# Kernel tuning notes

Measured on AMD Instinct MI355X. Metric: run time of the kernel, lower is better.

The kernel has to match this reference:

```python
import jax, jax.numpy as jnp
import numpy as np

B, N, Z = 32, 8192, 1024


def setup_inputs() -> dict:
    key = jax.random.key(0)
    ks = jax.random.split(key, 11)
    def w(k, shape, fan_in):
        # kaiming-ish init scale for conv1d k=1
        return jax.random.normal(k, shape, dtype=jnp.float32) * (1.0 / np.sqrt(fan_in))
    return {
        "x": jax.random.normal(ks[0], (B, 3, N), dtype=jnp.float32),
        "W1": w(ks[1], (64, 3), 3),   "b1": jnp.zeros((64,), jnp.float32),
        "W2": w(ks[2], (128, 64), 64), "b2": jnp.zeros((128,), jnp.float32),
        "W3": w(ks[3], (256, 128), 128), "b3": jnp.zeros((256,), jnp.float32),
        "W4": w(ks[4], (256, 256), 256), "b4": jnp.zeros((256,), jnp.float32),
        "W5": w(ks[5], (Z, 256), 256),  "b5": jnp.zeros((Z,), jnp.float32),
    }


def _pointwise(x, W, b):
    # Conv1d with kernel_size=1 == per-point linear: [B,C,N] x [O,C] -> [B,O,N]
    return jnp.einsum('bcn,oc->bon', x, W) + b[None, :, None]


def reference(x, W1, b1, W2, b2, W3, b3, W4, b4, W5, b5):
    h = jax.nn.relu(_pointwise(x, W1, b1))
    h = jax.nn.relu(_pointwise(h, W2, b2))
    h = jax.nn.relu(_pointwise(h, W3, b3))
    h = jax.nn.relu(_pointwise(h, W4, b4))
    h = _pointwise(h, W5, b5)           # [B, Z, N]
    return jnp.max(h, axis=2)           # global max pool over points -> [B, Z]
```

## Files before the change

### kernel.cpp

```cpp
#include <hip/hip_runtime.h>
#include <math.h>

#define NB      32
#define NPTS    8192
#define TOTPTS  (NB * NPTS)

typedef unsigned short u16;
typedef unsigned int   u32;
typedef __attribute__((ext_vector_type(8))) short bf16x8;
typedef __attribute__((ext_vector_type(4))) float f32x4;

__device__ __forceinline__ u16 f2bf(float f) {
    u32 u = __float_as_uint(f);
    u = (u + 0x7fffu + ((u >> 16) & 1u)) >> 16;
    return (u16)u;
}
__device__ __forceinline__ u32 pk2(float a, float b) {
    return (u32)f2bf(a) | ((u32)f2bf(b) << 16);
}
__device__ __forceinline__ f32x4 MFMA(bf16x8 a, bf16x8 b, f32x4 c) {
    return __builtin_amdgcn_mfma_f32_16x16x32_bf16(a, b, c, 0, 0, 0);
}
template<int CTRL>
__device__ __forceinline__ float dpp_max(float v) {
    int t = __builtin_amdgcn_update_dpp(__float_as_int(v), __float_as_int(v),
                                        CTRL, 0xF, 0xF, false);
    return fmaxf(v, __int_as_float(t));
}
__device__ __forceinline__ float rowmax16(float v) {
    v = dpp_max<0xB1>(v);
    v = dpp_max<0x4E>(v);
    v = dpp_max<0x141>(v);
    v = dpp_max<0x140>(v);
    return v;
}
__device__ __forceinline__ void gload16(const void* g, void* l) {
    __builtin_amdgcn_global_load_lds(
        (const __attribute__((address_space(1))) unsigned int*)g,
        (__attribute__((address_space(3))) unsigned int*)l, 16, 0, 0);
}
template<int N> __device__ __forceinline__ void vwait() {
    if constexpr      (N == 0) asm volatile("s_waitcnt vmcnt(0)" ::: "memory");
    else if constexpr (N == 2) asm volatile("s_waitcnt vmcnt(2)" ::: "memory");
    else if constexpr (N == 4) asm volatile("s_waitcnt vmcnt(4)" ::: "memory");
    else                       asm volatile("s_waitcnt vmcnt(8)" ::: "memory");
}
__device__ __forceinline__ void pin(bf16x8& v) { asm volatile("" : "+v"(v)); }


__global__ __launch_bounds__(256) void k_pack(const float* __restrict__ W2,
        const float* __restrict__ W3, const float* __restrict__ W4,
        const float* __restrict__ W5, u16* __restrict__ dst) {
    int idx = blockIdx.x * 256 + threadIdx.x;
    if (idx >= 720 * 64) return;
    int lane = idx & 63, fr = idx >> 6;
    const float* W; int C, frl;
    if (fr < 16)       { W = W2; C = 64;  frl = fr;       }
    else if (fr < 80)  { W = W3; C = 128; frl = fr - 16;  }
    else if (fr < 208) { W = W4; C = 256; frl = fr - 80;  }
    else               { W = W5; C = 256; frl = fr - 208; }
    int KF = C >> 5;
    int nf = frl / KF, kf = frl % KF;
    int o = nf * 16 + (lane & 15), c = kf * 32 + (lane >> 4) * 8;
    const float* s = W + (size_t)o * C + c;
    u32 out[4];
    #pragma unroll
    for (int j = 0; j < 4; ++j) out[j] = pk2(s[2 * j], s[2 * j + 1]);
    *(uint4*)((char*)dst + (size_t)idx * 16) = make_uint4(out[0], out[1], out[2], out[3]);
}

__global__ __launch_bounds__(512, 2) void k_fuse(const float* __restrict__ x,
        const float* __restrict__ W1, const float* __restrict__ b1,
        const u16* __restrict__ W2p, const float* __restrict__ b2,
        const u16* __restrict__ W3p, const float* __restrict__ b3,
        const u16* __restrict__ W4p, const float* __restrict__ b4,
        u16* __restrict__ H4, int pt0, int tpb) {
    __shared__ char regA[65536];
    __shared__ char regB[32768];
    const int tid = threadIdx.x, lane = tid & 63, w = tid >> 6;
    const int l15 = lane & 15, q = lane >> 4;
    const int qterm = ((q >> 1) * 16 + l15) * 16 + (q & 1) * 8;
    const int pl = tid & 127;
    const int c4 = tid >> 7;

    bf16x8 W2r[2], W3r[2][4], W4r[2][8];
    #pragma unroll
    for (int kf = 0; kf < 2; ++kf) {
        W2r[kf] = *(const bf16x8*)((const char*)W2p + (size_t)(w * 2 + kf) * 1024 + lane * 16);
        pin(W2r[kf]);
    }
    #pragma unroll
    for (int n = 0; n < 2; ++n)
        #pragma unroll
        for (int kf = 0; kf < 4; ++kf) {
            W3r[n][kf] = *(const bf16x8*)((const char*)W3p +
                           (size_t)((w * 2 + n) * 4 + kf) * 1024 + lane * 16);
            pin(W3r[n][kf]);
        }
    #pragma unroll
    for (int n = 0; n < 2; ++n)
        #pragma unroll
        for (int kf = 0; kf < 8; ++kf) {
            W4r[n][kf] = *(const bf16x8*)((const char*)W4p +
                           (size_t)((w * 2 + n) * 8 + kf) * 1024 + lane * 16);
            pin(W4r[n][kf]);
        }
    const f32x4 b2v = *(const f32x4*)(b2 + w * 16 + q * 4);
    f32x4 b3v[2], b4v[2];
    #pragma unroll
    for (int n = 0; n < 2; ++n) {
        b3v[n] = *(const f32x4*)(b3 + (w * 2 + n) * 16 + q * 4);
        b4v[n] = *(const f32x4*)(b4 + (w * 2 + n) * 16 + q * 4);
    }

    const int tile0 = blockIdx.x * tpb;
    float x0, x1, x2;
    {
        int ptg = pt0 + tile0 * 128 + pl;
        const float* xb = x + (size_t)(ptg >> 13) * 3 * NPTS + (ptg & 8191);
        x0 = xb[0]; x1 = xb[NPTS]; x2 = xb[2 * NPTS];
    }

    for (int it = 0; it < tpb; ++it) {
        const int tile = tile0 + it;
        {
            u32 pk4[8];
            #pragma unroll
            for (int i = 0; i < 8; ++i) {
                int o0 = c4 * 16 + 2 * i, o1 = o0 + 1;
                float a0 = fmaxf(b1[o0] + W1[o0*3]*x0 + W1[o0*3+1]*x1 + W1[o0*3+2]*x2, 0.f);
                float a1 = fmaxf(b1[o1] + W1[o1*3]*x0 + W1[o1*3+1]*x1 + W1[o1*3+2]*x2, 0.f);
                pk4[i] = pk2(a0, a1);
            }
            char* rowp = regA + pl * 128;
            const int swz = (pl & 7) << 4;
            *(uint4*)(rowp + ((c4 * 32) ^ swz))      = make_uint4(pk4[0], pk4[1], pk4[2], pk4[3]);
            *(uint4*)(rowp + ((c4 * 32 + 16) ^ swz)) = make_uint4(pk4[4], pk4[5], pk4[6], pk4[7]);
        }
        __syncthreads();
        #pragma unroll
        for (int pf = 0; pf < 8; ++pf) {
            const int r2 = pf * 16 + l15;
            const char* rb = regA + r2 * 128;
            const int rsw = (r2 & 7) << 4;
            bf16x8 B0 = *(const bf16x8*)(rb + ((q * 16) ^ rsw));
            bf16x8 B1 = *(const bf16x8*)(rb + ((64 + q * 16) ^ rsw));
            f32x4 a = b2v;
            a = MFMA(W2r[0], B0, a);
            a = MFMA(W2r[1], B1, a);
            u32 d0 = pk2(fmaxf(a[0], 0.f), fmaxf(a[1], 0.f));
            u32 d1 = pk2(fmaxf(a[2], 0.f), fmaxf(a[3], 0.f));
            *(uint2*)(regB + (pf * 4 + (w >> 1)) * 1024 + (w & 1) * 512 + qterm)
                = make_uint2(d0, d1);
        }
        __syncthreads();
        #pragma unroll
        for (int pf = 0; pf < 8; ++pf) {
            bf16x8 B[4];
            #pragma unroll
            for (int kf = 0; kf < 4; ++kf)
                B[kf] = *(const bf16x8*)(regB + (pf * 4 + kf) * 1024 + lane * 16);
            f32x4 a0 = b3v[0], a1 = b3v[1];
            #pragma unroll
            for (int kf = 0; kf < 4; ++kf) {
                a0 = MFMA(W3r[0][kf], B[kf], a0);
                a1 = MFMA(W3r[1][kf], B[kf], a1);
            }
            char* db = regA + (pf * 8 + w) * 1024;
            *(uint2*)(db + qterm)       = make_uint2(pk2(fmaxf(a0[0],0.f), fmaxf(a0[1],0.f)),
                                                     pk2(fmaxf(a0[2],0.f), fmaxf(a0[3],0.f)));
            *(uint2*)(db + 512 + qterm) = make_uint2(pk2(fmaxf(a1[0],0.f), fmaxf(a1[1],0.f)),
                                                     pk2(fmaxf(a1[2],0.f), fmaxf(a1[3],0.f)));
        }
        __syncthreads();
        #pragma unroll
        for (int pf = 0; pf < 8; ++pf) {
            bf16x8 B[8];
            #pragma unroll
            for (int kf = 0; kf < 8; ++kf)
                B[kf] = *(const bf16x8*)(regA + (pf * 8 + kf) * 1024 + lane * 16);
            f32x4 a0 = b4v[0], a1 = b4v[1];
            #pragma unroll
            for (int kf = 0; kf < 8; ++kf) {
                a0 = MFMA(W4r[0][kf], B[kf], a0);
                a1 = MFMA(W4r[1][kf], B[kf], a1);
            }
            char* db = (char*)H4 + ((size_t)(tile * 8 + pf) * 8 + w) * 1024;
            *(uint2*)(db + qterm)       = make_uint2(pk2(fmaxf(a0[0],0.f), fmaxf(a0[1],0.f)),
                                                     pk2(fmaxf(a0[2],0.f), fmaxf(a0[3],0.f)));
            *(uint2*)(db + 512 + qterm) = make_uint2(pk2(fmaxf(a1[0],0.f), fmaxf(a1[1],0.f)),
                                                     pk2(fmaxf(a1[2],0.f), fmaxf(a1[3],0.f)));
        }
        if (it + 1 < tpb) {
            int ptg = pt0 + (tile + 1) * 128 + pl;
            const float* xb = x + (size_t)(ptg >> 13) * 3 * NPTS + (ptg & 8191);
            x0 = xb[0]; x1 = xb[NPTS]; x2 = xb[2 * NPTS];
        }
        __syncthreads();
    }
}

__global__ __launch_bounds__(512, 2) void k_l5(const u16* __restrict__ Hin,
        const u16* __restrict__ Wp, const float* __restrict__ b5,
        float* __restrict__ parts, int slot0) {
    constexpr int BUFB = 16384;
    constexpr int STEPS = 32;
    __shared__ char ldsB[3 * BUFB];
    const int tid = threadIdx.x, lane = tid & 63, w = tid >> 6;
    const int l15 = lane & 15, q = lane >> 4;
    const int zsl = blockIdx.x & 1, pgrp = blockIdx.x >> 1;
    const int pfb = pgrp * 64;

    bf16x8 W[4][8];
    {
        const char* wb = (const char*)Wp + (size_t)(zsl * 32 + w * 4) * 8 * 1024;
        #pragma unroll
        for (int nf = 0; nf < 4; ++nf)
            #pragma unroll
            for (int kf = 0; kf < 8; ++kf)
                W[nf][kf] = *(const bf16x8*)(wb + (size_t)(nf * 8 + kf) * 1024 + lane * 16);
    }
    f32x4 vmax[4];
    #pragma unroll
    for (int nf = 0; nf < 4; ++nf)
        #pragma unroll
        for (int r = 0; r < 4; ++r) vmax[nf][r] = -3.402823466e38f;

    auto stage = [&](int t, int bsel) {
        const char* g = (const char*)Hin + ((size_t)(pfb + t * 2) * 8) * 1024
                        + w * 2048 + lane * 16;
        char* l = ldsB + bsel * BUFB + w * 2048;
        gload16(g, l);
        gload16(g + 1024, l + 1024);
    };
    stage(0, 0);
    stage(1, 1);
    int bufc = 0;
    for (int t = 0; t < STEPS; ++t) {
        if (t + 1 < STEPS) vwait<2>(); else vwait<0>();
        __builtin_amdgcn_sched_barrier(0);
        __builtin_amdgcn_s_barrier();
        const char* bp = ldsB + bufc * BUFB;
        #pragma unroll
        for (int p = 0; p < 2; ++p) {
            f32x4 acc[4];
            #pragma unroll
            for (int nf = 0; nf < 4; ++nf)
                #pragma unroll
                for (int r = 0; r < 4; ++r) acc[nf][r] = 0.f;
            #pragma unroll
            for (int kf = 0; kf < 8; ++kf) {
                bf16x8 B = *(const bf16x8*)(bp + (size_t)(p * 8 + kf) * 1024 + lane * 16);
                #pragma unroll
                for (int nf = 0; nf < 4; ++nf) acc[nf] = MFMA(W[nf][kf], B, acc[nf]);
            }
            #pragma unroll
            for (int nf = 0; nf < 4; ++nf)
                #pragma unroll
                for (int r = 0; r < 4; ++r)
                    vmax[nf][r] = fmaxf(vmax[nf][r], acc[nf][r]);
        }
        if (t + 2 < STEPS) {
            int b2 = bufc + 2; if (b2 >= 3) b2 -= 3;
            stage(t + 2, b2);
        }
        ++bufc; if (bufc == 3) bufc = 0;
    }
    const int zb = zsl * 512 + w * 64;
    float* dst = parts + (size_t)(slot0 + pgrp) * 1024 + zb;
    #pragma unroll
    for (int nf = 0; nf < 4; ++nf)
        #pragma unroll
        for (int r = 0; r < 4; ++r) {
            float m = rowmax16(vmax[nf][r]);
            if (l15 == nf * 4 + r) {
                int zi = nf * 16 + q * 4 + r;
                dst[zi] = m + b5[zb + zi];
            }
        }
}

__global__ __launch_bounds__(256) void k_red(const float* __restrict__ parts,
                                             float* __restrict__ out) {
    int i = blockIdx.x * 256 + threadIdx.x;
    int b = i >> 10, z = i & 1023;
    float m = -3.402823466e38f;
    #pragma unroll
    for (int s = 0; s < 8; ++s)
        m = fmaxf(m, parts[((size_t)b * 8 + s) * 1024 + z]);
    out[i] = m;
}

extern "C" void kernel_launch(void* const* d_in, const int* in_sizes, int n_in,
                              void* d_out, int out_size, void* d_ws, size_t ws_size,
                              hipStream_t stream) {
    const float* x  = (const float*)d_in[0];
    const float* W1 = (const float*)d_in[1]; const float* b1 = (const float*)d_in[2];
    const float* W2 = (const float*)d_in[3]; const float* b2 = (const float*)d_in[4];
    const float* W3 = (const float*)d_in[5]; const float* b3 = (const float*)d_in[6];
    const float* W4 = (const float*)d_in[7]; const float* b4 = (const float*)d_in[8];
    const float* W5 = (const float*)d_in[9]; const float* b5 = (const float*)d_in[10];

    u16* wsW = (u16*)d_ws;
    const u16* W2p = (const u16*)((char*)d_ws + 0);
    const u16* W3p = (const u16*)((char*)d_ws + 16 * 1024);
    const u16* W4p = (const u16*)((char*)d_ws + 80 * 1024);
    const u16* W5p = (const u16*)((char*)d_ws + 208 * 1024);
    float* parts   = (float*)((char*)d_ws + 786432);
    char* Hbase    = (char*)d_ws + 786432 + 2097152;

    int NCH = 1;
    while (NCH < 32) {
        size_t npc = (size_t)TOTPTS / NCH;
        if (786432 + 2097152 + npc * 512 <= ws_size) break;
        NCH *= 2;
    }
    const size_t npts_c = (size_t)TOTPTS / NCH;
    char* HB = Hbase;

    k_pack<<<dim3(180), dim3(256), 0, stream>>>(W2, W3, W4, W5, wsW);

    const int ntiles = (int)(npts_c / 128);
    const int nblk   = (ntiles >= 256) ? 256 : ntiles;
    const int tpb    = ntiles / nblk;
    const int npc_pf = (int)(npts_c / 16);
    for (int c = 0; c < NCH; ++c) {
        int pt0   = (int)(c * npts_c);
        int slot0 = (int)((c * npts_c) >> 10);
        k_fuse<<<dim3(nblk), dim3(512), 0, stream>>>(
            x, W1, b1, W2p, b2, W3p, b3, W4p, b4, (u16*)HB, pt0, tpb);
        k_l5<<<dim3(2 * (npc_pf / 64)), dim3(512), 0, stream>>>(
            (const u16*)HB, W5p, b5, parts, slot0);
    }
    k_red<<<dim3(128), dim3(256), 0, stream>>>(parts, (float*)d_out);
}
```

Baseline: 164.4 us.

## Switch layer-5 GEMM to 32x32x16 MFMA with matching H4 and W5 layouts

Layer 5 now uses the 32x32x16 bf16 MFMA instead of 16x16x32. The W5 packing, the H4 intermediate layout written by k_fuse, the staging addresses, and the final max reduction epilogue are all changed to fit the 32-wide fragment layout. The larger MFMA shape raises operand reuse per instruction and cuts LDS B-fragment reads per output tile. The cost is a more complex epilogue that needs cross-half shuffles, plus the chance of layout-index mistakes.

```diff
diff --git a/kernel.cpp b/kernel.cpp
--- a/kernel.cpp
+++ b/kernel.cpp
@@ -9,6 +9,7 @@
 typedef unsigned int   u32;
 typedef __attribute__((ext_vector_type(8))) short bf16x8;
 typedef __attribute__((ext_vector_type(4))) float f32x4;
+typedef __attribute__((ext_vector_type(16))) float f32x16;
 
 __device__ __forceinline__ u16 f2bf(float f) {
     u32 u = __float_as_uint(f);
@@ -20,6 +21,9 @@
 }
 __device__ __forceinline__ f32x4 MFMA(bf16x8 a, bf16x8 b, f32x4 c) {
     return __builtin_amdgcn_mfma_f32_16x16x32_bf16(a, b, c, 0, 0, 0);
+}
+__device__ __forceinline__ f32x16 MFMA32(bf16x8 a, bf16x8 b, f32x16 c) {
+    return __builtin_amdgcn_mfma_f32_32x32x16_bf16(a, b, c, 0, 0, 0);
 }
 template<int CTRL>
 __device__ __forceinline__ float dpp_max(float v) {
@@ -42,8 +46,7 @@
 template<int N> __device__ __forceinline__ void vwait() {
     if constexpr      (N == 0) asm volatile("s_waitcnt vmcnt(0)" ::: "memory");
     else if constexpr (N == 2) asm volatile("s_waitcnt vmcnt(2)" ::: "memory");
-    else if constexpr (N == 4) asm volatile("s_waitcnt vmcnt(4)" ::: "memory");
-    else                       asm volatile("s_waitcnt vmcnt(8)" ::: "memory");
+    else                       asm volatile("s_waitcnt vmcnt(4)" ::: "memory");
 }
 __device__ __forceinline__ void pin(bf16x8& v) { asm volatile("" : "+v"(v)); }
 
@@ -54,14 +57,23 @@
     int idx = blockIdx.x * 256 + threadIdx.x;
     if (idx >= 720 * 64) return;
     int lane = idx & 63, fr = idx >> 6;
-    const float* W; int C, frl;
-    if (fr < 16)       { W = W2; C = 64;  frl = fr;       }
-    else if (fr < 80)  { W = W3; C = 128; frl = fr - 16;  }
-    else if (fr < 208) { W = W4; C = 256; frl = fr - 80;  }
-    else               { W = W5; C = 256; frl = fr - 208; }
-    int KF = C >> 5;
-    int nf = frl / KF, kf = frl % KF;
-    int o = nf * 16 + (lane & 15), c = kf * 32 + (lane >> 4) * 8;
+    const float* W; int C, o, c;
+    if (fr < 208) {
+        int frl;
+        if (fr < 16)      { W = W2; C = 64;  frl = fr;      }
+        else if (fr < 80) { W = W3; C = 128; frl = fr - 16; }
+        else              { W = W4; C = 256; frl = fr - 80; }
+        int KF = C >> 5;
+        int nf = frl / KF, kf = frl % KF;
+        o = nf * 16 + (lane & 15);
+        c = kf * 32 + (lane >> 4) * 8;
+    } else {
+        int frl = fr - 208;
+        int nf = frl >> 4, kf = frl & 15;
+        W = W5; C = 256;
+        o = nf * 32 + (lane & 31);
+        c = kf * 16 + (lane >> 5) * 8;
+    }
     const float* s = W + (size_t)o * C + c;
     u32 out[4];
     #pragma unroll
@@ -185,11 +197,14 @@
                 a0 = MFMA(W4r[0][kf], B[kf], a0);
                 a1 = MFMA(W4r[1][kf], B[kf], a1);
             }
-            char* db = (char*)H4 + ((size_t)(tile * 8 + pf) * 8 + w) * 1024;
-            *(uint2*)(db + qterm)       = make_uint2(pk2(fmaxf(a0[0],0.f), fmaxf(a0[1],0.f)),
-                                                     pk2(fmaxf(a0[2],0.f), fmaxf(a0[3],0.f)));
-            *(uint2*)(db + 512 + qterm) = make_uint2(pk2(fmaxf(a1[0],0.f), fmaxf(a1[1],0.f)),
-                                                     pk2(fmaxf(a1[2],0.f), fmaxf(a1[3],0.f)));
+            const size_t pf32 = (size_t)tile * 4 + (pf >> 1);
+            const int lterm = ((q >> 1) * 32 + (pf & 1) * 16 + l15) * 16 + (q & 1) * 8;
+            char* d0p = (char*)H4 + (pf32 * 16 + (w * 2 + 0)) * 1024 + lterm;
+            char* d1p = (char*)H4 + (pf32 * 16 + (w * 2 + 1)) * 1024 + lterm;
+            *(uint2*)d0p = make_uint2(pk2(fmaxf(a0[0],0.f), fmaxf(a0[1],0.f)),
+                                      pk2(fmaxf(a0[2],0.f), fmaxf(a0[3],0.f)));
+            *(uint2*)d1p = make_uint2(pk2(fmaxf(a1[0],0.f), fmaxf(a1[1],0.f)),
+                                      pk2(fmaxf(a1[2],0.f), fmaxf(a1[3],0.f)));
         }
         if (it + 1 < tpb) {
             int ptg = pt0 + (tile + 1) * 128 + pl;
@@ -207,28 +222,24 @@
     constexpr int STEPS = 32;
     __shared__ char ldsB[3 * BUFB];
     const int tid = threadIdx.x, lane = tid & 63, w = tid >> 6;
-    const int l15 = lane & 15, q = lane >> 4;
     const int zsl = blockIdx.x & 1, pgrp = blockIdx.x >> 1;
-    const int pfb = pgrp * 64;
-
-    bf16x8 W[4][8];
+    const int pfb = pgrp * 32;
+
+    bf16x8 W[2][16];
     {
-        const char* wb = (const char*)Wp + (size_t)(zsl * 32 + w * 4) * 8 * 1024;
-        #pragma unroll
-        for (int nf = 0; nf < 4; ++nf)
-            #pragma unroll
-            for (int kf = 0; kf < 8; ++kf)
-                W[nf][kf] = *(const bf16x8*)(wb + (size_t)(nf * 8 + kf) * 1024 + lane * 16);
-    }
-    f32x4 vmax[4];
-    #pragma unroll
-    for (int nf = 0; nf < 4; ++nf)
-        #pragma unroll
-        for (int r = 0; r < 4; ++r) vmax[nf][r] = -3.402823466e38f;
+        const char* wb = (const char*)Wp + (size_t)(zsl * 16 + w * 2) * 16 * 1024;
+        #pragma unroll
+        for (int n = 0; n < 2; ++n)
+            #pragma unroll
+            for (int kf = 0; kf < 16; ++kf)
+                W[n][kf] = *(const bf16x8*)(wb + (size_t)(n * 16 + kf) * 1024 + lane * 16);
+    }
+    f32x16 vmax0, vmax1;
+    #pragma unroll
+    for (int r = 0; r < 16; ++r) { vmax0[r] = -3.402823466e38f; vmax1[r] = -3.402823466e38f; }
 
     auto stage = [&](int t, int bsel) {
-        const char* g = (const char*)Hin + ((size_t)(pfb + t * 2) * 8) * 1024
-                        + w * 2048 + lane * 16;
+        const char* g = (const char*)Hin + (size_t)(pfb + t) * 16384 + w * 2048 + lane * 16;
         char* l = ldsB + bsel * BUFB + w * 2048;
         gload16(g, l);
         gload16(g + 1024, l + 1024);
@@ -241,24 +252,19 @@
         __builtin_amdgcn_sched_barrier(0);
         __builtin_amdgcn_s_barrier();
         const char* bp = ldsB + bufc * BUFB;
-        #pragma unroll
-        for (int p = 0; p < 2; ++p) {
-            f32x4 acc[4];
-            #pragma unroll
-            for (int nf = 0; nf < 4; ++nf)
-                #pragma unroll
-                for (int r = 0; r < 4; ++r) acc[nf][r] = 0.f;
-            #pragma unroll
-            for (int kf = 0; kf < 8; ++kf) {
-                bf16x8 B = *(const bf16x8*)(bp + (size_t)(p * 8 + kf) * 1024 + lane * 16);
-                #pragma unroll
-                for (int nf = 0; nf < 4; ++nf) acc[nf] = MFMA(W[nf][kf], B, acc[nf]);
-            }
-            #pragma unroll
-            for (int nf = 0; nf < 4; ++nf)
-                #pragma unroll
-                for (int r = 0; r < 4; ++r)
-                    vmax[nf][r] = fmaxf(vmax[nf][r], acc[nf][r]);
+        f32x16 acc0, acc1;
+        #pragma unroll
+        for (int r = 0; r < 16; ++r) { acc0[r] = 0.f; acc1[r] = 0.f; }
+        #pragma unroll
+        for (int kf = 0; kf < 16; ++kf) {
+            bf16x8 B = *(const bf16x8*)(bp + (size_t)kf * 1024 + lane * 16);
+            acc0 = MFMA32(W[0][kf], B, acc0);
+            acc1 = MFMA32(W[1][kf], B, acc1);
+        }
+        #pragma unroll
+        for (int r = 0; r < 16; ++r) {
+            vmax0[r] = fmaxf(vmax0[r], acc0[r]);
+            vmax1[r] = fmaxf(vmax1[r], acc1[r]);
         }
         if (t + 2 < STEPS) {
             int b2 = bufc + 2; if (b2 >= 3) b2 -= 3;
@@ -267,17 +273,19 @@
         ++bufc; if (bufc == 3) bufc = 0;
     }
     const int zb = zsl * 512 + w * 64;
-    float* dst = parts + (size_t)(slot0 + pgrp) * 1024 + zb;
-    #pragma unroll
-    for (int nf = 0; nf < 4; ++nf)
-        #pragma unroll
-        for (int r = 0; r < 4; ++r) {
-            float m = rowmax16(vmax[nf][r]);
-            if (l15 == nf * 4 + r) {
-                int zi = nf * 16 + q * 4 + r;
-                dst[zi] = m + b5[zb + zi];
-            }
-        }
+    float mywr = -3.402823466e38f;
+    #pragma unroll
+    for (int r = 0; r < 16; ++r) {
+        float m0 = rowmax16(vmax0[r]);
+        m0 = fmaxf(m0, __shfl_xor(m0, 16, 64));
+        if ((lane & 31) == r) mywr = m0;
+        float m1 = rowmax16(vmax1[r]);
+        m1 = fmaxf(m1, __shfl_xor(m1, 16, 64));
+        if ((lane & 31) == 16 + r) mywr = m1;
+    }
+    const int r_ = lane & 15;
+    const int zloc = zb + ((lane >> 4) & 1) * 32 + (r_ & 3) + 8 * (r_ >> 2) + 4 * (lane >> 5);
+    parts[(size_t)(slot0 + pgrp) * 1024 + zloc] = mywr + b5[zloc];
 }
 
 __global__ __launch_bounds__(256) void k_red(const float* __restrict__ parts,
@@ -323,13 +331,12 @@
     const int ntiles = (int)(npts_c / 128);
     const int nblk   = (ntiles >= 256) ? 256 : ntiles;
     const int tpb    = ntiles / nblk;
-    const int npc_pf = (int)(npts_c / 16);
     for (int c = 0; c < NCH; ++c) {
         int pt0   = (int)(c * npts_c);
         int slot0 = (int)((c * npts_c) >> 10);
         k_fuse<<<dim3(nblk), dim3(512), 0, stream>>>(
             x, W1, b1, W2p, b2, W3p, b3, W4p, b4, (u16*)HB, pt0, tpb);
-        k_l5<<<dim3(2 * (npc_pf / 64)), dim3(512), 0, stream>>>(
+        k_l5<<<dim3(2 * (int)(npts_c / 1024)), dim3(512), 0, stream>>>(
             (const u16*)HB, W5p, b5, parts, slot0);
     }
     k_red<<<dim3(128), dim3(256), 0, stream>>>(parts, (float*)d_out);
```

Result: slower. 180.1 us (+9.6%).

## Give each wave a private double-buffered LDS stage in k_l5 and drop block barriers

Applied to the files above, without the earlier changes.

The layer-5 kernel used to share triple-buffered LDS tiles across all 8 waves and synchronise them with a workgroup barrier on every step. Now each wave loads its own copy of each point fragment into a private 16KB double buffer, so only per-wave vmcnt waits remain. Work per step drops to one fragment, with twice as many steps. It also pins the weight fragments to AGPRs, lowers launch bounds to one block per CU, and remaps block indices so the two z-slices of a point group run close together. In exchange, every wave now fetches the same data separately, which is eight times the global/L2 traffic for H4, and occupancy is halved.

```diff
diff --git a/kernel.cpp b/kernel.cpp
--- a/kernel.cpp
+++ b/kernel.cpp
@@ -45,7 +45,8 @@
     else if constexpr (N == 4) asm volatile("s_waitcnt vmcnt(4)" ::: "memory");
     else                       asm volatile("s_waitcnt vmcnt(8)" ::: "memory");
 }
-__device__ __forceinline__ void pin(bf16x8& v) { asm volatile("" : "+v"(v)); }
+__device__ __forceinline__ void pin(bf16x8& v)  { asm volatile("" : "+v"(v)); }
+__device__ __forceinline__ void pinA(bf16x8& v) { asm volatile("" : "+a"(v)); }
 
 
 __global__ __launch_bounds__(256) void k_pack(const float* __restrict__ W2,
@@ -200,16 +201,17 @@
     }
 }
 
-__global__ __launch_bounds__(512, 2) void k_l5(const u16* __restrict__ Hin,
+__global__ __launch_bounds__(512, 1) void k_l5(const u16* __restrict__ Hin,
         const u16* __restrict__ Wp, const float* __restrict__ b5,
         float* __restrict__ parts, int slot0) {
-    constexpr int BUFB = 16384;
-    constexpr int STEPS = 32;
-    __shared__ char ldsB[3 * BUFB];
+    constexpr int STEPS = 64;
+    __shared__ char ldsB[131072];
     const int tid = threadIdx.x, lane = tid & 63, w = tid >> 6;
     const int l15 = lane & 15, q = lane >> 4;
-    const int zsl = blockIdx.x & 1, pgrp = blockIdx.x >> 1;
-    const int pfb = pgrp * 64;
+    const int bid  = blockIdx.x;
+    const int zsl  = (bid >> 3) & 1;
+    const int pgrp = (bid & 7) | ((bid >> 4) << 3);
+    const int pfb  = pgrp * 64;
 
     bf16x8 W[4][8];
     {
@@ -217,8 +219,10 @@
         #pragma unroll
         for (int nf = 0; nf < 4; ++nf)
             #pragma unroll
-            for (int kf = 0; kf < 8; ++kf)
+            for (int kf = 0; kf < 8; ++kf) {
                 W[nf][kf] = *(const bf16x8*)(wb + (size_t)(nf * 8 + kf) * 1024 + lane * 16);
+                pinA(W[nf][kf]);
+            }
     }
     f32x4 vmax[4];
     #pragma unroll
@@ -226,45 +230,38 @@
         #pragma unroll
         for (int r = 0; r < 4; ++r) vmax[nf][r] = -3.402823466e38f;
 
+    char* myb = ldsB + w * 16384;
     auto stage = [&](int t, int bsel) {
-        const char* g = (const char*)Hin + ((size_t)(pfb + t * 2) * 8) * 1024
-                        + w * 2048 + lane * 16;
-        char* l = ldsB + bsel * BUFB + w * 2048;
-        gload16(g, l);
-        gload16(g + 1024, l + 1024);
+        const char* g = (const char*)Hin + ((size_t)(pfb + t) * 8) * 1024 + lane * 16;
+        char* l = myb + bsel * 8192;
+        #pragma unroll
+        for (int i = 0; i < 8; ++i)
+            gload16(g + i * 1024, l + i * 1024);
     };
     stage(0, 0);
     stage(1, 1);
-    int bufc = 0;
     for (int t = 0; t < STEPS; ++t) {
-        if (t + 1 < STEPS) vwait<2>(); else vwait<0>();
+        if (t < STEPS - 1) vwait<8>(); else vwait<0>();
         __builtin_amdgcn_sched_barrier(0);
-        __builtin_amdgcn_s_barrier();
-        const char* bp = ldsB + bufc * BUFB;
-        #pragma unroll
-        for (int p = 0; p < 2; ++p) {
-            f32x4 acc[4];
-            #pragma unroll
-            for (int nf = 0; nf < 4; ++nf)
-                #pragma unroll
-                for (int r = 0; r < 4; ++r) acc[nf][r] = 0.f;
-            #pragma unroll
-            for (int kf = 0; kf < 8; ++kf) {
-                bf16x8 B = *(const bf16x8*)(bp + (size_t)(p * 8 + kf) * 1024 + lane * 16);
-                #pragma unroll
-                for (int nf = 0; nf < 4; ++nf) acc[nf] = MFMA(W[nf][kf], B, acc[nf]);
-            }
-            #pragma unroll
-            for (int nf = 0; nf < 4; ++nf)
-                #pragma unroll
-                for (int r = 0; r < 4; ++r)
-                    vmax[nf][r] = fmaxf(vmax[nf][r], acc[nf][r]);
-        }
-        if (t + 2 < STEPS) {
-            int b2 = bufc + 2; if (b2 >= 3) b2 -= 3;
-            stage(t + 2, b2);
-        }
-        ++bufc; if (bufc == 3) bufc = 0;
+        const char* bp = myb + (t & 1) * 8192;
+        f32x4 acc[4];
+        #pragma unroll
+        for (int nf = 0; nf < 4; ++nf)
+            #pragma unroll
+            for (int r = 0; r < 4; ++r) acc[nf][r] = 0.f;
+        #pragma unroll
+        for (int kf = 0; kf < 8; ++kf) {
+            bf16x8 B = *(const bf16x8*)(bp + (size_t)kf * 1024 + lane * 16);
+            #pragma unroll
+            for (int nf = 0; nf < 4; ++nf) acc[nf] = MFMA(W[nf][kf], B, acc[nf]);
+        }
+        #pragma unroll
+        for (int nf = 0; nf < 4; ++nf)
+            #pragma unroll
+            for (int r = 0; r < 4; ++r)
+                vmax[nf][r] = fmaxf(vmax[nf][r], acc[nf][r]);
+        __builtin_amdgcn_sched_barrier(0);
+        if (t + 2 < STEPS) stage(t + 2, t & 1);
     }
     const int zb = zsl * 512 + w * 64;
     float* dst = parts + (size_t)(slot0 + pgrp) * 1024 + zb;
```

After: 203.6 us. 1.24x slower.
